# Performance work log

Hardware: AMD Instinct MI355X
Metric: run time of the kernel (lower is better)

The kernel has to match this reference:

```python
import jax, jax.numpy as jnp
import numpy as np

LAYERS, BLOCKS = 10, 3
N_BLK = LAYERS * BLOCKS
RC, SC, K = 128, 128, 2
IN_CH, COND_CH, OUT_CH = 256, 80, 256
DILATIONS = tuple(2 ** (i % LAYERS) for i in range(N_BLK))
INV_SQRT2 = 0.70710678118


def conv1x1(x, w, b):
    # x: [B, I, T], w: [O, I], b: [O] -> [B, O, T]
    return jnp.einsum('oi,bit->bot', w, x) + b[None, :, None]


def causal_conv(x, w, b, dilation):
    # x: [B, C, T], w: [O, I, K]; left-pad by (K-1)*d == torch pad-both + right slice
    pad = (w.shape[2] - 1) * dilation
    y = jax.lax.conv_general_dilated(
        x, w, window_strides=(1,), padding=[(pad, 0)],
        rhs_dilation=(dilation,), dimension_numbers=('NCH', 'OIH', 'NCH'))
    return y + b[None, :, None]


def setup_inputs() -> dict:
    key = jax.random.key(0)
    ks = jax.random.split(key, 20)
    s = 0.05
    B, T = 2, 8000
    inp = {
        'x': jax.random.normal(ks[0], (B, IN_CH, T), jnp.float32),
        'condition': jax.random.normal(ks[1], (B, COND_CH, T), jnp.float32),
        'input_w': jax.random.normal(ks[2], (RC, IN_CH), jnp.float32) * s,
        'input_b': jax.random.normal(ks[3], (RC,), jnp.float32) * s,
        'dil_w': jax.random.normal(ks[4], (N_BLK, RC, RC, K), jnp.float32) * s,
        'dil_b': jax.random.normal(ks[5], (N_BLK, RC), jnp.float32) * s,
        'gate_w': jax.random.normal(ks[6], (N_BLK, RC, RC), jnp.float32) * s,
        'gate_b': jax.random.normal(ks[7], (N_BLK, RC), jnp.float32) * s,
        'cond_w': jax.random.normal(ks[8], (N_BLK, RC, COND_CH), jnp.float32) * s,
        'cond_b': jax.random.normal(ks[9], (N_BLK, RC), jnp.float32) * s,
        'condg_w': jax.random.normal(ks[10], (N_BLK, RC, COND_CH), jnp.float32) * s,
        'condg_b': jax.random.normal(ks[11], (N_BLK, RC), jnp.float32) * s,
        'res_w': jax.random.normal(ks[12], (N_BLK, RC, RC), jnp.float32) * s,
        'res_b': jax.random.normal(ks[13], (N_BLK, RC), jnp.float32) * s,
        'skip_w': jax.random.normal(ks[14], (N_BLK, SC, RC), jnp.float32) * s,
        'skip_b': jax.random.normal(ks[15], (N_BLK, SC), jnp.float32) * s,
        'out1_w': jax.random.normal(ks[16], (SC, SC), jnp.float32) * s,
        'out1_b': jax.random.normal(ks[17], (SC,), jnp.float32) * s,
        'out2_w': jax.random.normal(ks[18], (OUT_CH, SC), jnp.float32) * s,
        'out2_b': jax.random.normal(ks[19], (OUT_CH,), jnp.float32) * s,
    }
    return inp


def reference(x, condition, input_w, input_b, dil_w, dil_b, gate_w, gate_b,
              cond_w, cond_b, condg_w, condg_b, res_w, res_b,
              skip_w, skip_b, out1_w, out1_b, out2_w, out2_b):
    h = conv1x1(x, input_w, input_b)  # [B, RC, T]
    skip = jnp.zeros_like(conv1x1(h, skip_w[0], skip_b[0]) * 0)  # [B, SC, T]
    for i, d in enumerate(DILATIONS):
        a = causal_conv(h, dil_w[i], dil_b[i], d) + conv1x1(condition, cond_w[i], cond_b[i])
        g = conv1x1(h, gate_w[i], gate_b[i]) + conv1x1(condition, condg_w[i], condg_b[i])
        out = jnp.tanh(a) * jax.nn.sigmoid(g)
        h = (h + conv1x1(out, res_w[i], res_b[i])) * INV_SQRT2
        skip = skip + conv1x1(out, skip_w[i], skip_b[i])
    y = jax.nn.relu(conv1x1(skip, out1_w, out1_b))
    return conv1x1(y, out2_w, out2_b)  # [B, 256, T]
```

## Files before the change

kernel.cpp:

```cpp
#include <hip/hip_runtime.h>

#define T_LEN 8000
#define NTPB 125
#define NBLK 250
#define NLAYER 30
#define GUARD 512
#define HROWS (GUARD + T_LEN)
#define SLAB (HROWS * 128)
#define INV_SQRT2 0.70710678118f

typedef short bf16x8 __attribute__((ext_vector_type(8)));
typedef unsigned uint2v __attribute__((ext_vector_type(2)));
typedef unsigned uint4v __attribute__((ext_vector_type(4)));
typedef float f32x4 __attribute__((ext_vector_type(4)));

#define R_HT  0
#define R_OUT 8192
#define R_CND 16384
#define WB0   22528
#define WB1   38912
#define LDS_SHORTS 55296

#define LS 106496
#define C1 16384
#define C2 32768
#define C3 49152
#define C4 57344
#define C5 73728
#define C6 90112
#define IN_OFF   3194880
#define OUT1_OFF 3227648
#define OUT2_OFF 3244032

__device__ __forceinline__ unsigned short f2bf_u(float f) {
    union { float f; unsigned u; } v; v.f = f;
    unsigned u = v.u + 0x7FFFu + ((v.u >> 16) & 1u);
    return (unsigned short)(u >> 16);
}
__device__ __forceinline__ short f2bf(float f) { return (short)f2bf_u(f); }

__device__ __forceinline__ unsigned cvtpk(float lo, float hi) {
    unsigned r;
    asm("v_cvt_pk_bf16_f32 %0, %1, %2" : "=v"(r) : "v"(lo), "v"(hi));
    return r;
}

__device__ __forceinline__ float gated_act(float av, float gv) {
    float e  = __expf(-2.f * fabsf(av));
    float th = (1.f - e) * __builtin_amdgcn_rcpf(1.f + e);
    th = (av < 0.f) ? -th : th;
    float sg = __builtin_amdgcn_rcpf(1.f + __expf(-gv));
    return th * sg;
}

__device__ __forceinline__ void ldg16_sc1(bf16x8* d, const short* p) {
    asm volatile("global_load_dwordx4 %0, %1, off sc1" : "=v"(*d) : "v"(p));
}
__device__ __forceinline__ void stg8_sc1(short* p, uint2v v) {
    asm volatile("global_store_dwordx2 %0, %1, off sc1" : : "v"(p), "v"(v) : "memory");
}
__device__ __forceinline__ void st_flag(int* p, int v) {
    __hip_atomic_store(p, v, __ATOMIC_RELAXED, __HIP_MEMORY_SCOPE_AGENT);
}
__device__ __forceinline__ void wait_ge(const int* p, int v) {
    while (__hip_atomic_load(p, __ATOMIC_RELAXED, __HIP_MEMORY_SCOPE_AGENT) < v)
        __builtin_amdgcn_s_sleep(1);
}

__device__ __forceinline__ f32x4 mfma_(bf16x8 a, bf16x8 b, f32x4 c) {
    return __builtin_amdgcn_mfma_f32_16x16x32_bf16(a, b, c, 0, 0, 0);
}

__device__ __forceinline__ void gload_lds16(const short* g, short* l) {
    __builtin_amdgcn_global_load_lds(
        (const __attribute__((address_space(1))) unsigned int*)g,
        (__attribute__((address_space(3))) unsigned int*)l, 16, 0, 0);
}
__device__ __forceinline__ void stageW2(const short* src, short* dst, int wv, int lane) {
    gload_lds16(src + wv * 512 + lane * 8, dst + wv * 512);
    gload_lds16(src + (16 + wv) * 512 + lane * 8, dst + (16 + wv) * 512);
}
__device__ __forceinline__ void stageW1(const short* src, short* dst, int wv, int lane) {
    gload_lds16(src + wv * 512 + lane * 8, dst + wv * 512);
}

template<int NP>
__device__ __forceinline__ void pairN(const short* wb, const short* sm, int boff,
                                      int ks0, int lg, int awoff,
                                      f32x4* ac0, f32x4* ac1)
{
#pragma unroll
    for (int p = 0; p < NP; ++p) {
        bf16x8 B = *(const bf16x8*)&sm[boff + ((ks0 + p) * 4 + lg) * 512];
#pragma unroll
        for (int mt = 0; mt < 2; ++mt) {
            bf16x8 a0 = *(const bf16x8*)&wb[p * 8192 + awoff + mt * 512];
            ac0[mt] = mfma_(a0, B, ac0[mt]);
            bf16x8 a1 = *(const bf16x8*)&wb[p * 8192 + 4096 + awoff + mt * 512];
            ac1[mt] = mfma_(a1, B, ac1[mt]);
        }
    }
}
template<int NP>
__device__ __forceinline__ void singleN(const short* wb, const short* sm, int boff,
                                        int ks0, int lg, int awoff, f32x4* ac)
{
#pragma unroll
    for (int p = 0; p < NP; ++p) {
        bf16x8 B = *(const bf16x8*)&sm[boff + ((ks0 + p) * 4 + lg) * 512];
#pragma unroll
        for (int mt = 0; mt < 2; ++mt) {
            bf16x8 a = *(const bf16x8*)&wb[p * 4096 + awoff + mt * 512];
            ac[mt] = mfma_(a, B, ac[mt]);
        }
    }
}

__global__ __launch_bounds__(256) void k_pack(
    const float* __restrict__ dil_w, const float* __restrict__ gate_w,
    const float* __restrict__ cond_w, const float* __restrict__ condg_w,
    const float* __restrict__ res_w, const float* __restrict__ skip_w,
    const float* __restrict__ input_w, const float* __restrict__ out1_w,
    const float* __restrict__ out2_w,
    const float* __restrict__ dil_b, const float* __restrict__ cond_b,
    const float* __restrict__ gate_b, const float* __restrict__ condg_b,
    short* __restrict__ wp, short* __restrict__ hbt, int* __restrict__ flg)
{
    int gid = blockIdx.x * 256 + threadIdx.x;
    if (gid < 512) flg[gid] = 0;
    {
        int g2 = gid - 512;
        if (g2 >= 0 && g2 < 262144) {
            unsigned* hb32 = (unsigned*)hbt;
            int slab = g2 >> 15, off = g2 & 32767;
            hb32[(size_t)slab * (SLAB / 2) + off] = 0u;
        }
    }
    if (gid >= 6400 * 64) return;
    int fid = gid >> 6, lane = gid & 63;
    int lr = lane & 15, lg = lane >> 4;
    float v[8];
    if (fid < 6240) {
        int layer = fid / 208;
        int r = fid - layer * 208;
        int kl = r >> 3, f = r & 7;
        int m = f * 16 + lr;
        size_t mi = (size_t)layer * 128 + m;
        int mat, ks;
        if      (kl < 8)  { mat = (kl & 1) ? 2 : 1; ks = kl >> 1; }
        else if (kl < 14) { mat = (kl & 1) ? 4 : 3; ks = (kl - 8) >> 1; }
        else if (kl < 18) { mat = 0; ks = kl - 14; }
        else              { mat = (kl & 1) ? 6 : 5; ks = (kl - 18) >> 1; }
        int kb = ks * 32 + lg * 8;
#pragma unroll
        for (int e = 0; e < 8; ++e) {
            int k = kb + e;
            float val;
            switch (mat) {
                case 0:  val = dil_w[(mi * 128 + k) * 2];     break;
                case 1:  val = dil_w[(mi * 128 + k) * 2 + 1]; break;
                case 2:  val = gate_w[mi * 128 + k]; break;
                case 3:  val = (k < 80) ? cond_w[mi * 80 + k]
                               : ((k == 80) ? dil_b[mi] + cond_b[mi] : 0.f); break;
                case 4:  val = (k < 80) ? condg_w[mi * 80 + k]
                               : ((k == 80) ? gate_b[mi] + condg_b[mi] : 0.f); break;
                case 5:  val = res_w[mi * 128 + k]; break;
                default: val = skip_w[mi * 128 + k]; break;
            }
            v[e] = val;
        }
    } else if (fid < 6304) {
        int f = fid - 6240; int ks = f >> 3, fr = f & 7;
        int m = fr * 16 + lr; int kb = ks * 32 + lg * 8;
#pragma unroll
        for (int e = 0; e < 8; ++e) v[e] = input_w[(size_t)m * 256 + kb + e];
    } else if (fid < 6336) {
        int f = fid - 6304; int ks = f >> 3, fr = f & 7;
        int m = fr * 16 + lr; int kb = ks * 32 + lg * 8;
#pragma unroll
        for (int e = 0; e < 8; ++e) v[e] = out1_w[(size_t)m * 128 + kb + e];
    } else {
        int f = fid - 6336; int mt = f & 15; int ks = f >> 4;
        int m = mt * 16 + lr; int kb = ks * 32 + lg * 8;
#pragma unroll
        for (int e = 0; e < 8; ++e) v[e] = out2_w[(size_t)m * 128 + kb + e];
    }
    short* dst = wp + (size_t)fid * 512 + lane * 8;
#pragma unroll
    for (int e = 0; e < 8; ++e) dst[e] = f2bf(v[e]);
}

__global__ __launch_bounds__(1024, 4) void k_wavenet(
    const float* __restrict__ x, const float* __restrict__ cond,
    const short* __restrict__ wp, short* __restrict__ hbt,
    const float* __restrict__ ib, const float* __restrict__ rbias,
    const float* __restrict__ sbias, const float* __restrict__ b1,
    const float* __restrict__ b2, float* __restrict__ outp,
    int* __restrict__ rdy, int* __restrict__ dn)
{
    __shared__ __align__(16) short sm[LDS_SHORTS];

    const int tid  = threadIdx.x;
    const int lane = tid & 63;
    const int wv   = __builtin_amdgcn_readfirstlane(tid >> 6);
    const int wm   = wv & 3;
    const int wn   = wv >> 2;
    const int lr   = lane & 15, lg = lane >> 4;
    const int bidx = blockIdx.x;
    const int b    = bidx / NTPB;
    const int ti   = bidx - b * NTPB;
    const int t0   = ti * 64;
    const int tl   = wn * 16 + lr;
    const int tg   = t0 + tl;
    const int tl8  = tl * 8;
    const int lane8 = lane * 8;
    const int awoff = wm * 1024 + lane8;
    const int chA  = wm * 32 + lg * 4;
    const int kbA  = wm * 4 + (lg >> 1);
    const int e0   = (lg & 1) * 4;

    stageW2(wp + IN_OFF, (short*)&sm[WB0], wv, lane);
    stageW2(wp + IN_OFF + 16384, (short*)&sm[WB1], wv, lane);
    {
        const float* xb = x + (size_t)b * 256 * T_LEN + t0 + lane;
#pragma unroll
        for (int it = 0; it < 2; ++it) {
            int kb = wv * 2 + it;
            unsigned pk[4];
#pragma unroll
            for (int e = 0; e < 4; ++e)
                pk[e] = cvtpk(xb[(size_t)(kb * 8 + 2 * e) * T_LEN],
                              xb[(size_t)(kb * 8 + 2 * e + 1) * T_LEN]);
            *(uint4v*)&sm[(kb * 64 + lane) * 8] = *(uint4v*)pk;
        }
        if (wv < 12) {
            const float* cb = cond + (size_t)b * 80 * T_LEN + t0 + lane;
            unsigned pk[4];
#pragma unroll
            for (int e = 0; e < 4; ++e) {
                int c0 = wv * 8 + 2 * e, c1 = c0 + 1;
                float v0 = (c0 < 80) ? cb[(size_t)c0 * T_LEN] : ((c0 == 80) ? 1.f : 0.f);
                float v1 = (c1 < 80) ? cb[(size_t)c1 * T_LEN] : 0.f;
                pk[e] = cvtpk(v0, v1);
            }
            *(uint4v*)&sm[R_CND + (wv * 64 + lane) * 8] = *(uint4v*)pk;
        }
    }
    __syncthreads();

    f32x4 hres[2] = {{0.f,0.f,0.f,0.f},{0.f,0.f,0.f,0.f}};
    {
        f32x4 acc[2] = {{0.f,0.f,0.f,0.f},{0.f,0.f,0.f,0.f}};
        singleN<4>((const short*)&sm[WB0], sm, tl8, 0, lg, awoff, acc);
        singleN<4>((const short*)&sm[WB1], sm, tl8, 4, lg, awoff, acc);
#pragma unroll
        for (int mt = 0; mt < 2; ++mt) {
            int cb0 = chA + mt * 16;
            f32x4 bv = {ib[cb0], ib[cb0 + 1], ib[cb0 + 2], ib[cb0 + 3]};
            hres[mt] = acc[mt] + bv;
        }
    }
    __syncthreads();
    {
        short* hrow = hbt + (size_t)b * SLAB + (size_t)(GUARD + tg) * 128 + chA;
#pragma unroll
        for (int mt = 0; mt < 2; ++mt) {
            uint2v hv = {cvtpk(hres[mt][0], hres[mt][1]), cvtpk(hres[mt][2], hres[mt][3])};
            stg8_sc1(hrow + mt * 16, hv);
            *(uint2v*)&sm[R_HT + ((kbA + mt * 2) * 64 + tl) * 8 + e0] = hv;
        }
    }
    asm volatile("s_waitcnt vmcnt(0)" ::: "memory");
    __syncthreads();
    if (tid == 0) st_flag(&rdy[bidx], 1);

    f32x4 skp[2] = {{0.f,0.f,0.f,0.f},{0.f,0.f,0.f,0.f}};

    for (int li = 0; li < NLAYER; ++li) {
        const int d   = 1 << (li % 10);
        const int ksh = (d + 63) >> 6;
        const short* wl  = wp + (size_t)li * LS;
        const short* hcb = hbt + (size_t)((li & 3) * 2 + b) * SLAB;
        short*       hnb = hbt + (size_t)(((li + 1) & 3) * 2 + b) * SLAB;

        stageW2(wl, (short*)&sm[WB0], wv, lane);
        __syncthreads();
        stageW2(wl + C1, (short*)&sm[WB1], wv, lane);
        f32x4 aa[2] = {{0.f,0.f,0.f,0.f},{0.f,0.f,0.f,0.f}};
        f32x4 ag[2] = {{0.f,0.f,0.f,0.f},{0.f,0.f,0.f,0.f}};
        pairN<2>((const short*)&sm[WB0], sm, R_HT + tl8, 0, lg, awoff, aa, ag);
        __syncthreads();
        stageW2(wl + C2, (short*)&sm[WB0], wv, lane);
        pairN<2>((const short*)&sm[WB1], sm, R_HT + tl8, 2, lg, awoff, aa, ag);
        __syncthreads();
        stageW1(wl + C3, (short*)&sm[WB1], wv, lane);
        pairN<2>((const short*)&sm[WB0], sm, R_CND + tl8, 0, lg, awoff, aa, ag);
        __syncthreads();
        stageW2(wl + C4, (short*)&sm[WB0], wv, lane);
        if (lane == 0 && ti >= ksh) wait_ge(&rdy[bidx - ksh], li + 1);
        bf16x8 Bg[4];
        {
            const short* hr = hcb + (size_t)(GUARD + tg - d) * 128 + lg * 8;
#pragma unroll
            for (int ks = 0; ks < 4; ++ks) ldg16_sc1(&Bg[ks], hr + ks * 32);
        }
        pairN<1>((const short*)&sm[WB1], sm, R_CND + tl8, 2, lg, awoff, aa, ag);
        __syncthreads();
        if (tid == 0) st_flag(&dn[bidx], li + 1);
        stageW2(wl + C5, (short*)&sm[WB1], wv, lane);
        {
#pragma unroll
            for (int ks = 0; ks < 4; ++ks) {
#pragma unroll
                for (int mt = 0; mt < 2; ++mt) {
                    bf16x8 a = *(const bf16x8*)&sm[WB0 + ks * 4096 + awoff + mt * 512];
                    aa[mt] = mfma_(a, Bg[ks], aa[mt]);
                }
            }
        }
#pragma unroll
        for (int mt = 0; mt < 2; ++mt) {
            uint2v ov = {cvtpk(gated_act(aa[mt][0], ag[mt][0]), gated_act(aa[mt][1], ag[mt][1])),
                         cvtpk(gated_act(aa[mt][2], ag[mt][2]), gated_act(aa[mt][3], ag[mt][3]))};
            *(uint2v*)&sm[R_OUT + ((kbA + mt * 2) * 64 + tl) * 8 + e0] = ov;
        }
        __syncthreads();
        stageW2(wl + C6, (short*)&sm[WB0], wv, lane);
        f32x4 ar[2]  = {{0.f,0.f,0.f,0.f},{0.f,0.f,0.f,0.f}};
        f32x4 as2[2] = {{0.f,0.f,0.f,0.f},{0.f,0.f,0.f,0.f}};
        pairN<2>((const short*)&sm[WB1], sm, R_OUT + tl8, 0, lg, awoff, ar, as2);
        __syncthreads();
        pairN<2>((const short*)&sm[WB0], sm, R_OUT + tl8, 2, lg, awoff, ar, as2);

        const float* rbl = rbias + li * 128 + chA;
        const float* sbl = sbias + li * 128 + chA;
#pragma unroll
        for (int mt = 0; mt < 2; ++mt) {
            f32x4 rbv = {rbl[mt*16], rbl[mt*16+1], rbl[mt*16+2], rbl[mt*16+3]};
            f32x4 sbv = {sbl[mt*16], sbl[mt*16+1], sbl[mt*16+2], sbl[mt*16+3]};
            skp[mt]  = skp[mt] + as2[mt] + sbv;
            hres[mt] = (hres[mt] + ar[mt] + rbv) * INV_SQRT2;
        }
        if (li < NLAYER - 1) {
            if (lane == 0 && li >= 3) {
                int d3 = 1 << ((li - 3) % 10);
                int k3 = (d3 + 63) >> 6;
                if (ti + k3 < NTPB) wait_ge(&dn[bidx + k3], li - 2);
            }
            short* hrow = hnb + (size_t)(GUARD + tg) * 128 + chA;
#pragma unroll
            for (int mt = 0; mt < 2; ++mt) {
                uint2v hv = {cvtpk(hres[mt][0], hres[mt][1]), cvtpk(hres[mt][2], hres[mt][3])};
                stg8_sc1(hrow + mt * 16, hv);
                *(uint2v*)&sm[R_HT + ((kbA + mt * 2) * 64 + tl) * 8 + e0] = hv;
            }
        }
        asm volatile("s_waitcnt vmcnt(0)" ::: "memory");
        __syncthreads();
        if (tid == 0 && li < NLAYER - 1) st_flag(&rdy[bidx], li + 2);
    }

#pragma unroll
    for (int mt = 0; mt < 2; ++mt) {
        uint2v sv = {cvtpk(skp[mt][0], skp[mt][1]), cvtpk(skp[mt][2], skp[mt][3])};
        *(uint2v*)&sm[R_HT + ((kbA + mt * 2) * 64 + tl) * 8 + e0] = sv;
    }
    stageW2(wp + OUT1_OFF, (short*)&sm[WB0], wv, lane);
    stageW2(wp + OUT2_OFF, (short*)&sm[WB1], wv, lane);
    __syncthreads();
    f32x4 ay[2] = {{0.f,0.f,0.f,0.f},{0.f,0.f,0.f,0.f}};
    singleN<4>((const short*)&sm[WB0], sm, R_HT + tl8, 0, lg, awoff, ay);
#pragma unroll
    for (int mt = 0; mt < 2; ++mt) {
        int cb0 = chA + mt * 16;
        float y0 = fmaxf(ay[mt][0] + b1[cb0],     0.f);
        float y1 = fmaxf(ay[mt][1] + b1[cb0 + 1], 0.f);
        float y2 = fmaxf(ay[mt][2] + b1[cb0 + 2], 0.f);
        float y3 = fmaxf(ay[mt][3] + b1[cb0 + 3], 0.f);
        uint2v yv = {cvtpk(y0, y1), cvtpk(y2, y3)};
        *(uint2v*)&sm[R_OUT + ((kbA + mt * 2) * 64 + tl) * 8 + e0] = yv;
    }
    __syncthreads();
    stageW2(wp + OUT2_OFF + 16384, (short*)&sm[WB0], wv, lane);
    f32x4 ao[4] = {{0.f,0.f,0.f,0.f},{0.f,0.f,0.f,0.f},
                   {0.f,0.f,0.f,0.f},{0.f,0.f,0.f,0.f}};
    {
        const short* wb = (const short*)&sm[WB1];
#pragma unroll
        for (int ksp = 0; ksp < 2; ++ksp) {
            bf16x8 B = *(const bf16x8*)&sm[R_OUT + tl8 + (ksp * 4 + lg) * 512];
#pragma unroll
            for (int mt = 0; mt < 4; ++mt) {
                int fg = 4 * wm + mt;
                bf16x8 A = *(const bf16x8*)&wb[(ksp * 2 + (fg >> 3)) * 4096 + (fg & 7) * 512 + lane8];
                ao[mt] = mfma_(A, B, ao[mt]);
            }
        }
    }
    __syncthreads();
    {
        const short* wb = (const short*)&sm[WB0];
#pragma unroll
        for (int ksp = 0; ksp < 2; ++ksp) {
            bf16x8 B = *(const bf16x8*)&sm[R_OUT + tl8 + ((2 + ksp) * 4 + lg) * 512];
#pragma unroll
            for (int mt = 0; mt < 4; ++mt) {
                int fg = 4 * wm + mt;
                bf16x8 A = *(const bf16x8*)&wb[(ksp * 2 + (fg >> 3)) * 4096 + (fg & 7) * 512 + lane8];
                ao[mt] = mfma_(A, B, ao[mt]);
            }
        }
    }
#pragma unroll
    for (int mt = 0; mt < 4; ++mt) {
        int ch2 = wm * 64 + mt * 16 + lg * 4;
        float* op = outp + ((size_t)(b * 256 + ch2)) * T_LEN + tg;
        op[0]         = ao[mt][0] + b2[ch2];
        op[T_LEN]     = ao[mt][1] + b2[ch2 + 1];
        op[2 * T_LEN] = ao[mt][2] + b2[ch2 + 2];
        op[3 * T_LEN] = ao[mt][3] + b2[ch2 + 3];
    }
}

extern "C" void kernel_launch(void* const* d_in, const int* in_sizes, int n_in,
                              void* d_out, int out_size, void* d_ws, size_t ws_size,
                              hipStream_t stream)
{
    const float* x       = (const float*)d_in[0];
    const float* cond    = (const float*)d_in[1];
    const float* input_w = (const float*)d_in[2];
    const float* input_b = (const float*)d_in[3];
    const float* dil_w   = (const float*)d_in[4];
    const float* dil_b   = (const float*)d_in[5];
    const float* gate_w  = (const float*)d_in[6];
    const float* gate_b  = (const float*)d_in[7];
    const float* cond_w  = (const float*)d_in[8];
    const float* cond_b  = (const float*)d_in[9];
    const float* condg_w = (const float*)d_in[10];
    const float* condg_b = (const float*)d_in[11];
    const float* res_w   = (const float*)d_in[12];
    const float* res_b   = (const float*)d_in[13];
    const float* skip_w  = (const float*)d_in[14];
    const float* skip_b  = (const float*)d_in[15];
    const float* out1_w  = (const float*)d_in[16];
    const float* out1_b  = (const float*)d_in[17];
    const float* out2_w  = (const float*)d_in[18];
    const float* out2_b  = (const float*)d_in[19];
    float* outp = (float*)d_out;

    short* wpk = (short*)d_ws;
    short* hbt = wpk + (size_t)6400 * 512;
    int*   flg = (int*)(hbt + (size_t)8 * SLAB);
    int*   rdy = flg;
    int*   dn  = flg + 256;

    k_pack<<<1600, 256, 0, stream>>>(dil_w, gate_w, cond_w, condg_w, res_w, skip_w,
                                     input_w, out1_w, out2_w,
                                     dil_b, cond_b, gate_b, condg_b, wpk, hbt, flg);

    void* args[] = {(void*)&x, (void*)&cond, (void*)&wpk, (void*)&hbt,
                    (void*)&input_b, (void*)&res_b, (void*)&skip_b,
                    (void*)&out1_b, (void*)&out2_b, (void*)&outp,
                    (void*)&rdy, (void*)&dn};
    (void)hipLaunchCooperativeKernel((void*)k_wavenet, dim3(NBLK), dim3(1024), args, 0, stream);
}
```

Before: 291.1 us.

## Switch to 32x32x16 MFMA tiles and halve threads per block

Replaces the 16x16x32 bf16 MFMA with the 32x32x16 variant, repacking all weights for the new fragment layout and rewriting the B-operand and output indexing. Each block now uses 512 threads (8 waves) where every wave covers a 32-channel by 32-timestep tile instead of 16x16 pieces. The aim is fewer MFMA issues and fewer LDS operand reads per FLOP, and fewer waves per barrier. The cost is larger accumulators (16 floats each) that raise register pressure, and fewer waves available to hide latency in the per-layer dependency chain.

```diff
diff --git a/kernel.cpp b/kernel.cpp
--- a/kernel.cpp
+++ b/kernel.cpp
@@ -13,6 +13,7 @@
 typedef unsigned uint2v __attribute__((ext_vector_type(2)));
 typedef unsigned uint4v __attribute__((ext_vector_type(4)));
 typedef float f32x4 __attribute__((ext_vector_type(4)));
+typedef float f32x16 __attribute__((ext_vector_type(16)));
 
 #define R_HT  0
 #define R_OUT 8192
@@ -44,7 +45,6 @@
     asm("v_cvt_pk_bf16_f32 %0, %1, %2" : "=v"(r) : "v"(lo), "v"(hi));
     return r;
 }
-
 __device__ __forceinline__ float gated_act(float av, float gv) {
     float e  = __expf(-2.f * fabsf(av));
     float th = (1.f - e) * __builtin_amdgcn_rcpf(1.f + e);
@@ -52,7 +52,6 @@
     float sg = __builtin_amdgcn_rcpf(1.f + __expf(-gv));
     return th * sg;
 }
-
 __device__ __forceinline__ void ldg16_sc1(bf16x8* d, const short* p) {
     asm volatile("global_load_dwordx4 %0, %1, off sc1" : "=v"(*d) : "v"(p));
 }
@@ -66,53 +65,56 @@
     while (__hip_atomic_load(p, __ATOMIC_RELAXED, __HIP_MEMORY_SCOPE_AGENT) < v)
         __builtin_amdgcn_s_sleep(1);
 }
-
-__device__ __forceinline__ f32x4 mfma_(bf16x8 a, bf16x8 b, f32x4 c) {
-    return __builtin_amdgcn_mfma_f32_16x16x32_bf16(a, b, c, 0, 0, 0);
-}
-
+__device__ __forceinline__ f32x16 mfma32(bf16x8 a, bf16x8 b, f32x16 c) {
+    return __builtin_amdgcn_mfma_f32_32x32x16_bf16(a, b, c, 0, 0, 0);
+}
+__device__ __forceinline__ f32x16 zero16() {
+    f32x16 z = {0.f,0.f,0.f,0.f,0.f,0.f,0.f,0.f,0.f,0.f,0.f,0.f,0.f,0.f,0.f,0.f};
+    return z;
+}
 __device__ __forceinline__ void gload_lds16(const short* g, short* l) {
     __builtin_amdgcn_global_load_lds(
         (const __attribute__((address_space(1))) unsigned int*)g,
         (__attribute__((address_space(3))) unsigned int*)l, 16, 0, 0);
 }
-__device__ __forceinline__ void stageW2(const short* src, short* dst, int wv, int lane) {
-    gload_lds16(src + wv * 512 + lane * 8, dst + wv * 512);
-    gload_lds16(src + (16 + wv) * 512 + lane * 8, dst + (16 + wv) * 512);
-}
-__device__ __forceinline__ void stageW1(const short* src, short* dst, int wv, int lane) {
-    gload_lds16(src + wv * 512 + lane * 8, dst + wv * 512);
+__device__ __forceinline__ void stage32(const short* src, short* dst, int wv, int lane) {
+#pragma unroll
+    for (int r = 0; r < 4; ++r) {
+        int s = (r * 8 + wv) * 512;
+        gload_lds16(src + s + lane * 8, dst + s);
+    }
+}
+__device__ __forceinline__ void stage16(const short* src, short* dst, int wv, int lane) {
+#pragma unroll
+    for (int r = 0; r < 2; ++r) {
+        int s = (r * 8 + wv) * 512;
+        gload_lds16(src + s + lane * 8, dst + s);
+    }
 }
 
 template<int NP>
-__device__ __forceinline__ void pairN(const short* wb, const short* sm, int boff,
-                                      int ks0, int lg, int awoff,
-                                      f32x4* ac0, f32x4* ac1)
+__device__ __forceinline__ void pair32(const short* wb, const short* sm, int breg,
+                                       int ks0, int boff, int awoff,
+                                       f32x16& acA, f32x16& acG)
 {
 #pragma unroll
     for (int p = 0; p < NP; ++p) {
-        bf16x8 B = *(const bf16x8*)&sm[boff + ((ks0 + p) * 4 + lg) * 512];
-#pragma unroll
-        for (int mt = 0; mt < 2; ++mt) {
-            bf16x8 a0 = *(const bf16x8*)&wb[p * 8192 + awoff + mt * 512];
-            ac0[mt] = mfma_(a0, B, ac0[mt]);
-            bf16x8 a1 = *(const bf16x8*)&wb[p * 8192 + 4096 + awoff + mt * 512];
-            ac1[mt] = mfma_(a1, B, ac1[mt]);
-        }
+        bf16x8 B = *(const bf16x8*)&sm[breg + (ks0 + p) * 1024 + boff];
+        bf16x8 a0 = *(const bf16x8*)&wb[p * 4096 + awoff];
+        acA = mfma32(a0, B, acA);
+        bf16x8 a1 = *(const bf16x8*)&wb[p * 4096 + 2048 + awoff];
+        acG = mfma32(a1, B, acG);
     }
 }
 template<int NP>
-__device__ __forceinline__ void singleN(const short* wb, const short* sm, int boff,
-                                        int ks0, int lg, int awoff, f32x4* ac)
+__device__ __forceinline__ void single32(const short* wb, const short* sm, int breg,
+                                         int ks0, int boff, int awoff, f32x16& ac)
 {
 #pragma unroll
     for (int p = 0; p < NP; ++p) {
-        bf16x8 B = *(const bf16x8*)&sm[boff + ((ks0 + p) * 4 + lg) * 512];
-#pragma unroll
-        for (int mt = 0; mt < 2; ++mt) {
-            bf16x8 a = *(const bf16x8*)&wb[p * 4096 + awoff + mt * 512];
-            ac[mt] = mfma_(a, B, ac[mt]);
-        }
+        bf16x8 B = *(const bf16x8*)&sm[breg + (ks0 + p) * 1024 + boff];
+        bf16x8 a = *(const bf16x8*)&wb[p * 2048 + awoff];
+        ac = mfma32(a, B, ac);
     }
 }
 
@@ -138,20 +140,19 @@
     }
     if (gid >= 6400 * 64) return;
     int fid = gid >> 6, lane = gid & 63;
-    int lr = lane & 15, lg = lane >> 4;
+    int l31 = lane & 31, hi = lane >> 5;
     float v[8];
     if (fid < 6240) {
         int layer = fid / 208;
-        int r = fid - layer * 208;
-        int kl = r >> 3, f = r & 7;
-        int m = f * 16 + lr;
+        int fr = fid - layer * 208;
+        int mat, ks, chf;
+        if (fr < 64)       { ks = fr >> 3; int rem = fr & 7;  mat = (rem < 4) ? 1 : 2; chf = rem & 3; }
+        else if (fr < 112) { int f2 = fr - 64;  ks = f2 >> 3; int rem = f2 & 7; mat = (rem < 4) ? 3 : 4; chf = rem & 3; }
+        else if (fr < 144) { int f2 = fr - 112; ks = f2 >> 2; chf = f2 & 3; mat = 0; }
+        else               { int f2 = fr - 144; ks = f2 >> 3; int rem = f2 & 7; mat = (rem < 4) ? 5 : 6; chf = rem & 3; }
+        int m = chf * 32 + l31;
         size_t mi = (size_t)layer * 128 + m;
-        int mat, ks;
-        if      (kl < 8)  { mat = (kl & 1) ? 2 : 1; ks = kl >> 1; }
-        else if (kl < 14) { mat = (kl & 1) ? 4 : 3; ks = (kl - 8) >> 1; }
-        else if (kl < 18) { mat = 0; ks = kl - 14; }
-        else              { mat = (kl & 1) ? 6 : 5; ks = (kl - 18) >> 1; }
-        int kb = ks * 32 + lg * 8;
+        int kb = ks * 16 + hi * 8;
 #pragma unroll
         for (int e = 0; e < 8; ++e) {
             int k = kb + e;
@@ -170,18 +171,18 @@
             v[e] = val;
         }
     } else if (fid < 6304) {
-        int f = fid - 6240; int ks = f >> 3, fr = f & 7;
-        int m = fr * 16 + lr; int kb = ks * 32 + lg * 8;
+        int f = fid - 6240; int ks = f >> 2, chf = f & 3;
+        int m = chf * 32 + l31; int kb = ks * 16 + hi * 8;
 #pragma unroll
         for (int e = 0; e < 8; ++e) v[e] = input_w[(size_t)m * 256 + kb + e];
     } else if (fid < 6336) {
-        int f = fid - 6304; int ks = f >> 3, fr = f & 7;
-        int m = fr * 16 + lr; int kb = ks * 32 + lg * 8;
+        int f = fid - 6304; int ks = f >> 2, chf = f & 3;
+        int m = chf * 32 + l31; int kb = ks * 16 + hi * 8;
 #pragma unroll
         for (int e = 0; e < 8; ++e) v[e] = out1_w[(size_t)m * 128 + kb + e];
     } else {
-        int f = fid - 6336; int mt = f & 15; int ks = f >> 4;
-        int m = mt * 16 + lr; int kb = ks * 32 + lg * 8;
+        int f = fid - 6336; int ks = f >> 3, chf = f & 7;
+        int m = chf * 32 + l31; int kb = ks * 16 + hi * 8;
 #pragma unroll
         for (int e = 0; e < 8; ++e) v[e] = out2_w[(size_t)m * 128 + kb + e];
     }
@@ -190,7 +191,7 @@
     for (int e = 0; e < 8; ++e) dst[e] = f2bf(v[e]);
 }
 
-__global__ __launch_bounds__(1024, 4) void k_wavenet(
+__global__ __launch_bounds__(512, 2) void k_wavenet(
     const float* __restrict__ x, const float* __restrict__ cond,
     const short* __restrict__ wp, short* __restrict__ hbt,
     const float* __restrict__ ib, const float* __restrict__ rbias,
@@ -204,28 +205,27 @@
     const int lane = tid & 63;
     const int wv   = __builtin_amdgcn_readfirstlane(tid >> 6);
     const int wm   = wv & 3;
-    const int wn   = wv >> 2;
-    const int lr   = lane & 15, lg = lane >> 4;
+    const int wt   = wv >> 2;
+    const int l31  = lane & 31;
+    const int hi   = lane >> 5;
     const int bidx = blockIdx.x;
     const int b    = bidx / NTPB;
     const int ti   = bidx - b * NTPB;
     const int t0   = ti * 64;
-    const int tl   = wn * 16 + lr;
-    const int tg   = t0 + tl;
-    const int tl8  = tl * 8;
+    const int tloc = wt * 32 + l31;
+    const int tg   = t0 + tloc;
     const int lane8 = lane * 8;
-    const int awoff = wm * 1024 + lane8;
-    const int chA  = wm * 32 + lg * 4;
-    const int kbA  = wm * 4 + (lg >> 1);
-    const int e0   = (lg & 1) * 4;
-
-    stageW2(wp + IN_OFF, (short*)&sm[WB0], wv, lane);
-    stageW2(wp + IN_OFF + 16384, (short*)&sm[WB1], wv, lane);
+    const int awoff = wm * 512 + lane8;
+    const int boff  = hi * 512 + tloc * 8;
+    const int chW   = wm * 32 + 4 * hi;
+
+    stage32(wp + IN_OFF, (short*)&sm[WB0], wv, lane);
+    stage32(wp + IN_OFF + 16384, (short*)&sm[WB1], wv, lane);
     {
         const float* xb = x + (size_t)b * 256 * T_LEN + t0 + lane;
 #pragma unroll
-        for (int it = 0; it < 2; ++it) {
-            int kb = wv * 2 + it;
+        for (int it = 0; it < 4; ++it) {
+            int kb = wv * 4 + it;
             unsigned pk[4];
 #pragma unroll
             for (int e = 0; e < 4; ++e)
@@ -233,48 +233,51 @@
                               xb[(size_t)(kb * 8 + 2 * e + 1) * T_LEN]);
             *(uint4v*)&sm[(kb * 64 + lane) * 8] = *(uint4v*)pk;
         }
-        if (wv < 12) {
+        if (wv < 6) {
             const float* cb = cond + (size_t)b * 80 * T_LEN + t0 + lane;
-            unsigned pk[4];
-#pragma unroll
-            for (int e = 0; e < 4; ++e) {
-                int c0 = wv * 8 + 2 * e, c1 = c0 + 1;
-                float v0 = (c0 < 80) ? cb[(size_t)c0 * T_LEN] : ((c0 == 80) ? 1.f : 0.f);
-                float v1 = (c1 < 80) ? cb[(size_t)c1 * T_LEN] : 0.f;
-                pk[e] = cvtpk(v0, v1);
-            }
-            *(uint4v*)&sm[R_CND + (wv * 64 + lane) * 8] = *(uint4v*)pk;
+#pragma unroll
+            for (int it = 0; it < 2; ++it) {
+                int kb = wv * 2 + it;
+                unsigned pk[4];
+#pragma unroll
+                for (int e = 0; e < 4; ++e) {
+                    int c0 = kb * 8 + 2 * e, c1 = c0 + 1;
+                    float v0 = (c0 < 80) ? cb[(size_t)c0 * T_LEN] : ((c0 == 80) ? 1.f : 0.f);
+                    float v1 = (c1 < 80) ? cb[(size_t)c1 * T_LEN] : 0.f;
+                    pk[e] = cvtpk(v0, v1);
+                }
+                *(uint4v*)&sm[R_CND + (kb * 64 + lane) * 8] = *(uint4v*)pk;
+            }
         }
     }
     __syncthreads();
 
-    f32x4 hres[2] = {{0.f,0.f,0.f,0.f},{0.f,0.f,0.f,0.f}};
-    {
-        f32x4 acc[2] = {{0.f,0.f,0.f,0.f},{0.f,0.f,0.f,0.f}};
-        singleN<4>((const short*)&sm[WB0], sm, tl8, 0, lg, awoff, acc);
-        singleN<4>((const short*)&sm[WB1], sm, tl8, 4, lg, awoff, acc);
-#pragma unroll
-        for (int mt = 0; mt < 2; ++mt) {
-            int cb0 = chA + mt * 16;
-            f32x4 bv = {ib[cb0], ib[cb0 + 1], ib[cb0 + 2], ib[cb0 + 3]};
-            hres[mt] = acc[mt] + bv;
-        }
-    }
-    __syncthreads();
-    {
-        short* hrow = hbt + (size_t)b * SLAB + (size_t)(GUARD + tg) * 128 + chA;
-#pragma unroll
-        for (int mt = 0; mt < 2; ++mt) {
-            uint2v hv = {cvtpk(hres[mt][0], hres[mt][1]), cvtpk(hres[mt][2], hres[mt][3])};
-            stg8_sc1(hrow + mt * 16, hv);
-            *(uint2v*)&sm[R_HT + ((kbA + mt * 2) * 64 + tl) * 8 + e0] = hv;
+    f32x16 hres;
+    {
+        f32x16 acc = zero16();
+        single32<8>((const short*)&sm[WB0], sm, 0, 0, boff, awoff, acc);
+        single32<8>((const short*)&sm[WB1], sm, 0, 8, boff, awoff, acc);
+        __syncthreads();
+        const float* ibp = ib + chW;
+#pragma unroll
+        for (int q = 0; q < 4; ++q) {
+            f32x4 bv = *(const f32x4*)&ibp[8 * q];
+#pragma unroll
+            for (int j = 0; j < 4; ++j) hres[4 * q + j] = acc[4 * q + j] + bv[j];
+        }
+        short* hrow = hbt + (size_t)b * SLAB + (size_t)(GUARD + tg) * 128 + chW;
+#pragma unroll
+        for (int q = 0; q < 4; ++q) {
+            uint2v hv = {cvtpk(hres[4*q], hres[4*q+1]), cvtpk(hres[4*q+2], hres[4*q+3])};
+            stg8_sc1(hrow + 8 * q, hv);
+            *(uint2v*)&sm[R_HT + ((wm * 4 + q) * 64 + tloc) * 8 + 4 * hi] = hv;
         }
     }
     asm volatile("s_waitcnt vmcnt(0)" ::: "memory");
     __syncthreads();
     if (tid == 0) st_flag(&rdy[bidx], 1);
 
-    f32x4 skp[2] = {{0.f,0.f,0.f,0.f},{0.f,0.f,0.f,0.f}};
+    f32x16 skp = zero16();
 
     for (int li = 0; li < NLAYER; ++li) {
         const int d   = 1 << (li % 10);
@@ -283,63 +286,69 @@
         const short* hcb = hbt + (size_t)((li & 3) * 2 + b) * SLAB;
         short*       hnb = hbt + (size_t)(((li + 1) & 3) * 2 + b) * SLAB;
 
-        stageW2(wl, (short*)&sm[WB0], wv, lane);
-        __syncthreads();
-        stageW2(wl + C1, (short*)&sm[WB1], wv, lane);
-        f32x4 aa[2] = {{0.f,0.f,0.f,0.f},{0.f,0.f,0.f,0.f}};
-        f32x4 ag[2] = {{0.f,0.f,0.f,0.f},{0.f,0.f,0.f,0.f}};
-        pairN<2>((const short*)&sm[WB0], sm, R_HT + tl8, 0, lg, awoff, aa, ag);
-        __syncthreads();
-        stageW2(wl + C2, (short*)&sm[WB0], wv, lane);
-        pairN<2>((const short*)&sm[WB1], sm, R_HT + tl8, 2, lg, awoff, aa, ag);
-        __syncthreads();
-        stageW1(wl + C3, (short*)&sm[WB1], wv, lane);
-        pairN<2>((const short*)&sm[WB0], sm, R_CND + tl8, 0, lg, awoff, aa, ag);
-        __syncthreads();
-        stageW2(wl + C4, (short*)&sm[WB0], wv, lane);
+        stage32(wl, (short*)&sm[WB0], wv, lane);
+        __syncthreads();
+        stage32(wl + C1, (short*)&sm[WB1], wv, lane);
+        f32x16 aa = zero16(), ag = zero16();
+        pair32<4>((const short*)&sm[WB0], sm, R_HT, 0, boff, awoff, aa, ag);
+        __syncthreads();
+        stage32(wl + C2, (short*)&sm[WB0], wv, lane);
+        pair32<4>((const short*)&sm[WB1], sm, R_HT, 4, boff, awoff, aa, ag);
+        __syncthreads();
+        stage16(wl + C3, (short*)&sm[WB1], wv, lane);
+        pair32<4>((const short*)&sm[WB0], sm, R_CND, 0, boff, awoff, aa, ag);
+        __syncthreads();
+        stage32(wl + C4, (short*)&sm[WB0], wv, lane);
         if (lane == 0 && ti >= ksh) wait_ge(&rdy[bidx - ksh], li + 1);
-        bf16x8 Bg[4];
+        bf16x8 Bg[8];
         {
-            const short* hr = hcb + (size_t)(GUARD + tg - d) * 128 + lg * 8;
-#pragma unroll
-            for (int ks = 0; ks < 4; ++ks) ldg16_sc1(&Bg[ks], hr + ks * 32);
-        }
-        pairN<1>((const short*)&sm[WB1], sm, R_CND + tl8, 2, lg, awoff, aa, ag);
+            const short* hr = hcb + (size_t)(GUARD + tg - d) * 128 + hi * 8;
+#pragma unroll
+            for (int ks = 0; ks < 8; ++ks) ldg16_sc1(&Bg[ks], hr + ks * 16);
+        }
+        pair32<2>((const short*)&sm[WB1], sm, R_CND, 4, boff, awoff, aa, ag);
         __syncthreads();
         if (tid == 0) st_flag(&dn[bidx], li + 1);
-        stageW2(wl + C5, (short*)&sm[WB1], wv, lane);
+        stage32(wl + C5, (short*)&sm[WB1], wv, lane);
         {
-#pragma unroll
-            for (int ks = 0; ks < 4; ++ks) {
-#pragma unroll
-                for (int mt = 0; mt < 2; ++mt) {
-                    bf16x8 a = *(const bf16x8*)&sm[WB0 + ks * 4096 + awoff + mt * 512];
-                    aa[mt] = mfma_(a, Bg[ks], aa[mt]);
+            const short* wb = (const short*)&sm[WB0];
+#pragma unroll
+            for (int ks = 0; ks < 8; ++ks) {
+                bf16x8 a = *(const bf16x8*)&wb[ks * 2048 + awoff];
+                aa = mfma32(a, Bg[ks], aa);
+            }
+        }
+        {
+            float o[16];
+#pragma unroll
+            for (int i = 0; i < 16; ++i) o[i] = gated_act(aa[i], ag[i]);
+#pragma unroll
+            for (int q = 0; q < 4; ++q) {
+                uint2v ov = {cvtpk(o[4*q], o[4*q+1]), cvtpk(o[4*q+2], o[4*q+3])};
+                *(uint2v*)&sm[R_OUT + ((wm * 4 + q) * 64 + tloc) * 8 + 4 * hi] = ov;
+            }
+        }
+        __syncthreads();
+        stage32(wl + C6, (short*)&sm[WB0], wv, lane);
+        f32x16 ar = zero16(), as2 = zero16();
+        pair32<4>((const short*)&sm[WB1], sm, R_OUT, 0, boff, awoff, ar, as2);
+        __syncthreads();
+        pair32<4>((const short*)&sm[WB0], sm, R_OUT, 4, boff, awoff, ar, as2);
+
+        {
+            const float* rbl = rbias + li * 128 + chW;
+            const float* sbl = sbias + li * 128 + chW;
+#pragma unroll
+            for (int q = 0; q < 4; ++q) {
+                f32x4 rbv = *(const f32x4*)&rbl[8 * q];
+                f32x4 sbv = *(const f32x4*)&sbl[8 * q];
+#pragma unroll
+                for (int j = 0; j < 4; ++j) {
+                    int i = 4 * q + j;
+                    skp[i]  = skp[i] + as2[i] + sbv[j];
+                    hres[i] = (hres[i] + ar[i] + rbv[j]) * INV_SQRT2;
                 }
             }
-        }
-#pragma unroll
-        for (int mt = 0; mt < 2; ++mt) {
-            uint2v ov = {cvtpk(gated_act(aa[mt][0], ag[mt][0]), gated_act(aa[mt][1], ag[mt][1])),
-                         cvtpk(gated_act(aa[mt][2], ag[mt][2]), gated_act(aa[mt][3], ag[mt][3]))};
-            *(uint2v*)&sm[R_OUT + ((kbA + mt * 2) * 64 + tl) * 8 + e0] = ov;
-        }
-        __syncthreads();
-        stageW2(wl + C6, (short*)&sm[WB0], wv, lane);
-        f32x4 ar[2]  = {{0.f,0.f,0.f,0.f},{0.f,0.f,0.f,0.f}};
-        f32x4 as2[2] = {{0.f,0.f,0.f,0.f},{0.f,0.f,0.f,0.f}};
-        pairN<2>((const short*)&sm[WB1], sm, R_OUT + tl8, 0, lg, awoff, ar, as2);
-        __syncthreads();
-        pairN<2>((const short*)&sm[WB0], sm, R_OUT + tl8, 2, lg, awoff, ar, as2);
-
-        const float* rbl = rbias + li * 128 + chA;
-        const float* sbl = sbias + li * 128 + chA;
-#pragma unroll
-        for (int mt = 0; mt < 2; ++mt) {
-            f32x4 rbv = {rbl[mt*16], rbl[mt*16+1], rbl[mt*16+2], rbl[mt*16+3]};
-            f32x4 sbv = {sbl[mt*16], sbl[mt*16+1], sbl[mt*16+2], sbl[mt*16+3]};
-            skp[mt]  = skp[mt] + as2[mt] + sbv;
-            hres[mt] = (hres[mt] + ar[mt] + rbv) * INV_SQRT2;
         }
         if (li < NLAYER - 1) {
             if (lane == 0 && li >= 3) {
@@ -347,12 +356,12 @@
                 int k3 = (d3 + 63) >> 6;
                 if (ti + k3 < NTPB) wait_ge(&dn[bidx + k3], li - 2);
             }
-            short* hrow = hnb + (size_t)(GUARD + tg) * 128 + chA;
-#pragma unroll
-            for (int mt = 0; mt < 2; ++mt) {
-                uint2v hv = {cvtpk(hres[mt][0], hres[mt][1]), cvtpk(hres[mt][2], hres[mt][3])};
-                stg8_sc1(hrow + mt * 16, hv);
-                *(uint2v*)&sm[R_HT + ((kbA + mt * 2) * 64 + tl) * 8 + e0] = hv;
+            short* hrow = hnb + (size_t)(GUARD + tg) * 128 + chW;
+#pragma unroll
+            for (int q = 0; q < 4; ++q) {
+                uint2v hv = {cvtpk(hres[4*q], hres[4*q+1]), cvtpk(hres[4*q+2], hres[4*q+3])};
+                stg8_sc1(hrow + 8 * q, hv);
+                *(uint2v*)&sm[R_HT + ((wm * 4 + q) * 64 + tloc) * 8 + 4 * hi] = hv;
             }
         }
         asm volatile("s_waitcnt vmcnt(0)" ::: "memory");
@@ -361,64 +370,62 @@
     }
 
 #pragma unroll
-    for (int mt = 0; mt < 2; ++mt) {
-        uint2v sv = {cvtpk(skp[mt][0], skp[mt][1]), cvtpk(skp[mt][2], skp[mt][3])};
-        *(uint2v*)&sm[R_HT + ((kbA + mt * 2) * 64 + tl) * 8 + e0] = sv;
-    }
-    stageW2(wp + OUT1_OFF, (short*)&sm[WB0], wv, lane);
-    stageW2(wp + OUT2_OFF, (short*)&sm[WB1], wv, lane);
+    for (int q = 0; q < 4; ++q) {
+        uint2v sv = {cvtpk(skp[4*q], skp[4*q+1]), cvtpk(skp[4*q+2], skp[4*q+3])};
+        *(uint2v*)&sm[R_HT + ((wm * 4 + q) * 64 + tloc) * 8 + 4 * hi] = sv;
+    }
+    stage32(wp + OUT1_OFF, (short*)&sm[WB0], wv, lane);
+    stage32(wp + OUT2_OFF, (short*)&sm[WB1], wv, lane);
     __syncthreads();
-    f32x4 ay[2] = {{0.f,0.f,0.f,0.f},{0.f,0.f,0.f,0.f}};
-    singleN<4>((const short*)&sm[WB0], sm, R_HT + tl8, 0, lg, awoff, ay);
-#pragma unroll
-    for (int mt = 0; mt < 2; ++mt) {
-        int cb0 = chA + mt * 16;
-        float y0 = fmaxf(ay[mt][0] + b1[cb0],     0.f);
-        float y1 = fmaxf(ay[mt][1] + b1[cb0 + 1], 0.f);
-        float y2 = fmaxf(ay[mt][2] + b1[cb0 + 2], 0.f);
-        float y3 = fmaxf(ay[mt][3] + b1[cb0 + 3], 0.f);
-        uint2v yv = {cvtpk(y0, y1), cvtpk(y2, y3)};
-        *(uint2v*)&sm[R_OUT + ((kbA + mt * 2) * 64 + tl) * 8 + e0] = yv;
+    f32x16 ay = zero16();
+    single32<8>((const short*)&sm[WB0], sm, R_HT, 0, boff, awoff, ay);
+    {
+        const float* b1p = b1 + chW;
+#pragma unroll
+        for (int q = 0; q < 4; ++q) {
+            f32x4 bv = *(const f32x4*)&b1p[8 * q];
+            float y0 = fmaxf(ay[4*q]   + bv[0], 0.f);
+            float y1 = fmaxf(ay[4*q+1] + bv[1], 0.f);
+            float y2 = fmaxf(ay[4*q+2] + bv[2], 0.f);
+            float y3 = fmaxf(ay[4*q+3] + bv[3], 0.f);
+            uint2v yv = {cvtpk(y0, y1), cvtpk(y2, y3)};
+            *(uint2v*)&sm[R_OUT + ((wm * 4 + q) * 64 + tloc) * 8 + 4 * hi] = yv;
+        }
     }
     __syncthreads();
-    stageW2(wp + OUT2_OFF + 16384, (short*)&sm[WB0], wv, lane);
-    f32x4 ao[4] = {{0.f,0.f,0.f,0.f},{0.f,0.f,0.f,0.f},
-                   {0.f,0.f,0.f,0.f},{0.f,0.f,0.f,0.f}};
+    stage32(wp + OUT2_OFF + 16384, (short*)&sm[WB0], wv, lane);
+    f32x16 ao0 = zero16(), ao1 = zero16();
     {
         const short* wb = (const short*)&sm[WB1];
 #pragma unroll
-        for (int ksp = 0; ksp < 2; ++ksp) {
-            bf16x8 B = *(const bf16x8*)&sm[R_OUT + tl8 + (ksp * 4 + lg) * 512];
-#pragma unroll
-            for (int mt = 0; mt < 4; ++mt) {
-                int fg = 4 * wm + mt;
-                bf16x8 A = *(const bf16x8*)&wb[(ksp * 2 + (fg >> 3)) * 4096 + (fg & 7) * 512 + lane8];
-                ao[mt] = mfma_(A, B, ao[mt]);
-            }
+        for (int p = 0; p < 4; ++p) {
+            bf16x8 B = *(const bf16x8*)&sm[R_OUT + p * 1024 + boff];
+            bf16x8 a0 = *(const bf16x8*)&wb[p * 4096 + wm * 512 + lane8];
+            ao0 = mfma32(a0, B, ao0);
+            bf16x8 a1 = *(const bf16x8*)&wb[p * 4096 + (wm + 4) * 512 + lane8];
+            ao1 = mfma32(a1, B, ao1);
         }
     }
     __syncthreads();
     {
         const short* wb = (const short*)&sm[WB0];
 #pragma unroll
-        for (int ksp = 0; ksp < 2; ++ksp) {
-            bf16x8 B = *(const bf16x8*)&sm[R_OUT + tl8 + ((2 + ksp) * 4 + lg) * 512];
-#pragma unroll
-            for (int mt = 0; mt < 4; ++mt) {
-                int fg = 4 * wm + mt;
-                bf16x8 A = *(const bf16x8*)&wb[(ksp * 2 + (fg >> 3)) * 4096 + (fg & 7) * 512 + lane8];
-                ao[mt] = mfma_(A, B, ao[mt]);
-            }
-        }
-    }
-#pragma unroll
-    for (int mt = 0; mt < 4; ++mt) {
-        int ch2 = wm * 64 + mt * 16 + lg * 4;
-        float* op = outp + ((size_t)(b * 256 + ch2)) * T_LEN + tg;
-        op[0]         = ao[mt][0] + b2[ch2];
-        op[T_LEN]     = ao[mt][1] + b2[ch2 + 1];
-        op[2 * T_LEN] = ao[mt][2] + b2[ch2 + 2];
-        op[3 * T_LEN] = ao[mt][3] + b2[ch2 + 3];
+        for (int p = 0; p < 4; ++p) {
+            bf16x8 B = *(const bf16x8*)&sm[R_OUT + (4 + p) * 1024 + boff];
+            bf16x8 a0 = *(const bf16x8*)&wb[p * 4096 + wm * 512 + lane8];
+            ao0 = mfma32(a0, B, ao0);
+            bf16x8 a1 = *(const bf16x8*)&wb[p * 4096 + (wm + 4) * 512 + lane8];
+            ao1 = mfma32(a1, B, ao1);
+        }
+    }
+#pragma unroll
+    for (int q = 0; q < 4; ++q) {
+#pragma unroll
+        for (int j = 0; j < 4; ++j) {
+            int ch = chW + 8 * q + j;
+            outp[((size_t)(b * 256 + ch)) * T_LEN + tg]       = ao0[4*q+j] + b2[ch];
+            outp[((size_t)(b * 256 + ch + 128)) * T_LEN + tg] = ao1[4*q+j] + b2[ch + 128];
+        }
     }
 }
 
@@ -462,5 +469,5 @@
                     (void*)&input_b, (void*)&res_b, (void*)&skip_b,
                     (void*)&out1_b, (void*)&out2_b, (void*)&outp,
                     (void*)&rdy, (void*)&dn};
-    (void)hipLaunchCooperativeKernel((void*)k_wavenet, dim3(NBLK), dim3(1024), args, 0, stream);
-}
+    (void)hipLaunchCooperativeKernel((void*)k_wavenet, dim3(NBLK), dim3(512), args, 0, stream);
+}
```

Result: slower. 339.4 us (+16.6%).
